# Kernel optimization log

Hardware: AMD Instinct MI355X
Metric: run time of the kernel (lower is better)

Reference implementation:

```python
import jax, jax.numpy as jnp
import numpy as np

R = 3          # bilateral radius -> 7x7 window (kernel_size=7, dilation=1)
NIC = 12       # num_input_channels per frame
NHS = 1        # num_hidden_states
DN = ('NCHW', 'OIHW', 'NCHW')


def _conv(x, w, b, groups=1):
    y = jax.lax.conv_general_dilated(x, w, (1, 1), 'SAME',
                                     dimension_numbers=DN,
                                     feature_group_count=groups)
    return y + b[None, :, None, None]


def _lcn(x, k=3):
    # run_lcn(color, 3): local contrast normalization with k x k box window, per channel
    C = x.shape[1]
    box = jnp.ones((C, 1, k, k), x.dtype) / (k * k)
    zb = jnp.zeros((C,), x.dtype)
    mean = _conv(x, box, zb, groups=C)
    mean2 = _conv(x * x, box, zb, groups=C)
    var = jnp.maximum(mean2 - mean * mean, 0.0)
    return (x - mean) * jax.lax.rsqrt(var + 1e-5)


def _bilateral(dyn, feat, scale):
    # cross-bilateral: weights from guide features, applied to dynamic channels
    B, _, H, W = dyn.shape
    pad = ((0, 0), (0, 0), (R, R), (R, R))
    fp = jnp.pad(feat, pad, mode='edge')
    dp = jnp.pad(dyn, pad, mode='edge')
    s = scale[None, :, None, None]            # [1,8,1,1] per-feature inverse sigma^2
    acc = jnp.zeros_like(dyn)
    wsum = jnp.zeros((B, 1, H, W), dyn.dtype)
    for dy in range(2 * R + 1):
        for dx in range(2 * R + 1):
            fq = fp[:, :, dy:dy + H, dx:dx + W]
            w = jnp.exp(-jnp.sum(s * (feat - fq) ** 2, axis=1, keepdims=True))
            acc = acc + w * dp[:, :, dy:dy + H, dx:dx + W]
            wsum = wsum + w
    return acc / (wsum + 1e-8)


def _forward(x, alpha, cr_w0, cr_b0, cr_w1, cr_b1, cr_w2, cr_b2,
             hs_w0, hs_b0, hs_w1, hs_b1, hs_w2, hs_b2,
             filt_w, filt_b, filt_scale):
    B, CT, H, W = x.shape
    num_frames = CT // NIC
    a = alpha[0]
    temporal = jnp.zeros((B, 3 + NHS, H, W), x.dtype)
    outs = []
    for i in range(num_frames):
        frame = x[:, i * NIC:(i + 1) * NIC]
        color, albedo, fixed = frame[:, :3], frame[:, 3:6], frame[:, 3:]
        rec_in = jnp.concatenate([_lcn(color), color], axis=1)           # 6ch
        h = jax.nn.relu(_conv(rec_in, cr_w0, cr_b0))
        h = jax.nn.relu(_conv(h, cr_w1, cr_b1))
        recombined = _conv(h, cr_w2, cr_b2)                              # 3ch
        hs_in = jnp.concatenate([recombined, fixed], axis=1)             # 12ch
        h = jax.nn.relu(_conv(hs_in, hs_w0, hs_b0))
        h = jax.nn.relu(_conv(h, hs_w1, hs_b1))
        hidden = _conv(h, hs_w2, hs_b2)                                  # 1ch
        dynamic = jnp.concatenate([color, hidden], axis=1)               # 4ch
        if i != 0:
            dynamic = a * dynamic + (1.0 - a) * temporal
        filtered = jnp.concatenate([dynamic, fixed], axis=1)             # 13ch
        for k in range(5):
            feat = _conv(filtered, filt_w[k], filt_b[k])                 # 8 guide features
            fdyn = _bilateral(filtered[:, :3 + NHS], feat, filt_scale[k])
            filtered = jnp.concatenate([fdyn, fixed], axis=1)
        outs.append(albedo * filtered[:, :3])
        temporal = filtered[:, :3 + NHS]
    return jnp.concatenate(outs, axis=1)   # [B, 3*num_frames, H, W]


def setup_inputs():
    key = jax.random.key(0)
    ks = jax.random.split(key, 12)
    w = lambda k, s: (0.1 * jax.random.normal(k, s)).astype(jnp.float32)
    z = lambda s: jnp.zeros(s, jnp.float32)
    return {
        'x': jax.random.normal(ks[0], (1, 48, 720, 1280), dtype=jnp.float32),
        'alpha': jnp.full((1,), 0.5, jnp.float32),
        'cr_w0': w(ks[1], (6, 6, 3, 3)),   'cr_b0': z((6,)),
        'cr_w1': w(ks[2], (12, 6, 3, 3)),  'cr_b1': z((12,)),
        'cr_w2': w(ks[3], (3, 12, 3, 3)),  'cr_b2': z((3,)),
        'hs_w0': w(ks[4], (12, 12, 3, 3)), 'hs_b0': z((12,)),
        'hs_w1': w(ks[5], (12, 12, 3, 3)), 'hs_b1': z((12,)),
        'hs_w2': w(ks[6], (1, 12, 3, 3)),  'hs_b2': z((1,)),
        'filt_w': w(ks[7], (5, 8, 13, 3, 3)), 'filt_b': z((5, 8)),
        'filt_scale': 0.5 * jax.random.uniform(ks[8], (5, 8), dtype=jnp.float32),
    }


def reference(x, alpha, cr_w0, cr_b0, cr_w1, cr_b1, cr_w2, cr_b2,
              hs_w0, hs_b0, hs_w1, hs_b1, hs_w2, hs_b2,
              filt_w, filt_b, filt_scale):
    return _forward(x, alpha, cr_w0, cr_b0, cr_w1, cr_b1, cr_w2, cr_b2,
                    hs_w0, hs_b0, hs_w1, hs_b1, hs_w2, hs_b2,
                    filt_w, filt_b, filt_scale)
```

## Files before the change

kernel.cpp:

```cpp
#include <hip/hip_runtime.h>

#define HH 720
#define WW 1280
#define HWP (HH*WW)

static constexpr int NFRM = 4;
typedef _Float16 h2 __attribute__((ext_vector_type(2)));

template <int PX, int C0, int C1, int COUT, bool RELU>
__global__ __launch_bounds__(128) void conv3x3_v3(const float* __restrict__ in0, long i0fs,
                                                  const float* __restrict__ in1, long i1fs,
                                                  const float* __restrict__ w,
                                                  const float* __restrict__ b,
                                                  float* __restrict__ out, long ofs) {
  constexpr int CIN = C0 + C1;
  constexpr int NBX = WW / (16 * PX);
  int fi = blockIdx.y;
  in0 += (size_t)fi * i0fs;
  out += (size_t)fi * ofs;
  const float* in1f = nullptr;
  if constexpr (C1 > 0) in1f = in1 + (size_t)fi * i1fs;

  int bx = blockIdx.x % NBX;
  int by = blockIdx.x / NBX;
  int tx = threadIdx.x & 15;
  int ty = threadIdx.x >> 4;
  int gx0 = bx * (16 * PX) + tx * PX;
  int gy  = by * 8 + ty;

  float acc[COUT][PX];
  #pragma unroll
  for (int co = 0; co < COUT; ++co) {
    float bv = b[co];
    #pragma unroll
    for (int px = 0; px < PX; ++px) acc[co][px] = bv;
  }

  const bool lok = (gx0 > 0);
  const bool rok = (gx0 + PX < WW);

  for (int c = 0; c < CIN; ++c) {
    const float* ch;
    if constexpr (C1 > 0)
      ch = (c < C0) ? (in0 + (size_t)c * HWP) : (in1f + (size_t)(c - C0) * HWP);
    else
      ch = in0 + (size_t)c * HWP;
    float r[3][PX + 2];
    #pragma unroll
    for (int ky = 0; ky < 3; ++ky) {
      int iy = gy + ky - 1;
      bool yok = (iy >= 0) && (iy < HH);
      const float* row = ch + (ptrdiff_t)iy * WW;
      #pragma unroll
      for (int j = 0; j < PX / 4; ++j) {
        float4 a = yok ? *reinterpret_cast<const float4*>(row + gx0 + 4 * j)
                       : make_float4(0.f, 0.f, 0.f, 0.f);
        r[ky][1 + 4*j + 0] = a.x; r[ky][1 + 4*j + 1] = a.y;
        r[ky][1 + 4*j + 2] = a.z; r[ky][1 + 4*j + 3] = a.w;
      }
      r[ky][0]      = (yok && lok) ? row[gx0 - 1]  : 0.f;
      r[ky][PX + 1] = (yok && rok) ? row[gx0 + PX] : 0.f;
    }
    #pragma unroll
    for (int co = 0; co < COUT; ++co) {
      #pragma unroll
      for (int ky = 0; ky < 3; ++ky) {
        #pragma unroll
        for (int kx = 0; kx < 3; ++kx) {
          float wv = w[((co * CIN + c) * 3 + ky) * 3 + kx];
          #pragma unroll
          for (int px = 0; px < PX; ++px)
            acc[co][px] = fmaf(wv, r[ky][px + kx], acc[co][px]);
        }
      }
    }
  }

  size_t p = (size_t)gy * WW + gx0;
  #pragma unroll
  for (int co = 0; co < COUT; ++co) {
    #pragma unroll
    for (int j = 0; j < PX / 4; ++j) {
      float4 o;
      o.x = RELU ? fmaxf(acc[co][4*j+0], 0.f) : acc[co][4*j+0];
      o.y = RELU ? fmaxf(acc[co][4*j+1], 0.f) : acc[co][4*j+1];
      o.z = RELU ? fmaxf(acc[co][4*j+2], 0.f) : acc[co][4*j+2];
      o.w = RELU ? fmaxf(acc[co][4*j+3], 0.f) : acc[co][4*j+3];
      *reinterpret_cast<float4*>(out + (size_t)co * HWP + p + 4*j) = o;
    }
  }
}

__global__ __launch_bounds__(128) void lcn_v3(const float* __restrict__ x, long ifs,
                                              float* __restrict__ out, long ofs) {
  constexpr int NBX = WW / 128;
  int fi = blockIdx.y;
  const float* color = x + (size_t)fi * ifs;
  out += (size_t)fi * ofs;
  int bx = blockIdx.x % NBX;
  int by = blockIdx.x / NBX;
  int tx = threadIdx.x & 15;
  int ty = threadIdx.x >> 4;
  int gx0 = bx * 128 + tx * 8;
  int gy  = by * 8 + ty;
  const bool lok = (gx0 > 0);
  const bool rok = (gx0 + 8 < WW);
  size_t p = (size_t)gy * WW + gx0;

  #pragma unroll
  for (int c = 0; c < 3; ++c) {
    const float* ch = color + (size_t)c * HWP;
    float r[3][10];
    #pragma unroll
    for (int ky = 0; ky < 3; ++ky) {
      int iy = gy + ky - 1;
      bool yok = (iy >= 0) && (iy < HH);
      const float* row = ch + (ptrdiff_t)iy * WW;
      float4 a = yok ? *reinterpret_cast<const float4*>(row + gx0)
                     : make_float4(0.f, 0.f, 0.f, 0.f);
      float4 q = yok ? *reinterpret_cast<const float4*>(row + gx0 + 4)
                     : make_float4(0.f, 0.f, 0.f, 0.f);
      r[ky][0] = (yok && lok) ? row[gx0 - 1] : 0.f;
      r[ky][1] = a.x; r[ky][2] = a.y; r[ky][3] = a.z; r[ky][4] = a.w;
      r[ky][5] = q.x; r[ky][6] = q.y; r[ky][7] = q.z; r[ky][8] = q.w;
      r[ky][9] = (yok && rok) ? row[gx0 + 8] : 0.f;
    }
    float lcnv[8], cv[8];
    #pragma unroll
    for (int px = 0; px < 8; ++px) {
      float s = 0.f, s2 = 0.f;
      #pragma unroll
      for (int ky = 0; ky < 3; ++ky)
        #pragma unroll
        for (int kx = 0; kx < 3; ++kx) {
          float v = r[ky][px + kx];
          s += v; s2 = fmaf(v, v, s2);
        }
      float mean = s * (1.f / 9.f);
      float mean2 = s2 * (1.f / 9.f);
      float var = fmaxf(mean2 - mean * mean, 0.f);
      cv[px] = r[1][px + 1];
      lcnv[px] = (cv[px] - mean) * rsqrtf(var + 1e-5f);
    }
    #pragma unroll
    for (int h = 0; h < 2; ++h) {
      float4 o0 = make_float4(lcnv[4*h+0], lcnv[4*h+1], lcnv[4*h+2], lcnv[4*h+3]);
      float4 o1 = make_float4(cv[4*h+0], cv[4*h+1], cv[4*h+2], cv[4*h+3]);
      *reinterpret_cast<float4*>(out + (size_t)c * HWP + p + 4*h) = o0;
      *reinterpret_cast<float4*>(out + (size_t)(3 + c) * HWP + p + 4*h) = o1;
    }
  }
}

__global__ __launch_bounds__(256) void blend_v3(const float* __restrict__ color,
                                                const float* __restrict__ hid,
                                                const float* __restrict__ temporal,
                                                const float* __restrict__ alpha,
                                                float* __restrict__ dyn, int first) {
  int i = (blockIdx.x * 256 + threadIdx.x) * 4;
  if (i >= HWP) return;
  if (first) {
    #pragma unroll
    for (int c = 0; c < 3; ++c)
      *reinterpret_cast<float4*>(dyn + (size_t)c * HWP + i) =
          *reinterpret_cast<const float4*>(color + (size_t)c * HWP + i);
    *reinterpret_cast<float4*>(dyn + 3 * (size_t)HWP + i) =
        *reinterpret_cast<const float4*>(hid + i);
  } else {
    float a = alpha[0];
    float om = 1.f - a;
    #pragma unroll
    for (int c = 0; c < 4; ++c) {
      const float* src = (c < 3) ? (color + (size_t)c * HWP) : hid;
      float4 cv = *reinterpret_cast<const float4*>(src + i);
      float4 tv = *reinterpret_cast<const float4*>(temporal + (size_t)c * HWP + i);
      float4 o;
      o.x = a * cv.x + om * tv.x;
      o.y = a * cv.y + om * tv.y;
      o.z = a * cv.z + om * tv.z;
      o.w = a * cv.w + om * tv.w;
      *reinterpret_cast<float4*>(dyn + (size_t)c * HWP + i) = o;
    }
  }
}

#define BC 38
#define BR 22
#define BNPX (BC*BR)
#define BPAD 840

__device__ __forceinline__ int bswz(int lin) { return lin ^ ((lin >> 3) & 7); }
__device__ __forceinline__ unsigned pkh(float a, float b) {
  return __builtin_bit_cast(unsigned, __builtin_amdgcn_cvt_pkrtz(a, b));
}

template <bool OUT>
__global__ __launch_bounds__(256, 4) void bilateral_v5(const float* __restrict__ dyn,
                                                       const float* __restrict__ feat,
                                                       const float* __restrict__ scale,
                                                       float* __restrict__ outdyn,
                                                       const float* __restrict__ albedo,
                                                       float* __restrict__ outp) {
  __shared__ uint4  ft[BPAD];
  __shared__ float4 dt[BPAD];
  int bx = blockIdx.x % 40;
  int by = blockIdx.x / 40;
  int tid = threadIdx.x;

  for (int i = tid; i < BNPX; i += 256) {
    int py = i / BC;
    int px = i - py * BC;
    int gy = min(max(by * 16 + py - 3, 0), HH - 1);
    int gx = min(max(bx * 32 + px - 3, 0), WW - 1);
    size_t g = (size_t)gy * WW + gx;
    int w = bswz(i);
    dt[w] = make_float4(dyn[g], dyn[HWP + g], dyn[2*(size_t)HWP + g], dyn[3*(size_t)HWP + g]);
    uint4 u;
    u.x = pkh(feat[g],                 feat[HWP + g]);
    u.y = pkh(feat[2*(size_t)HWP + g], feat[3*(size_t)HWP + g]);
    u.z = pkh(feat[4*(size_t)HWP + g], feat[5*(size_t)HWP + g]);
    u.w = pkh(feat[6*(size_t)HWP + g], feat[7*(size_t)HWP + g]);
    ft[w] = u;
  }
  __syncthreads();

  int txg = tid & 15;
  int ty  = tid >> 4;

  float sv[8];
  #pragma unroll
  for (int c = 0; c < 8; ++c) sv[c] = scale[c];

  float sfc[2][8], A[2];
  #pragma unroll
  for (int p = 0; p < 2; ++p) {
    int lin = (ty + 3) * BC + txg * 2 + 3 + p;
    uint4 u = ft[bswz(lin)];
    h2 a0 = __builtin_bit_cast(h2, u.x), a1 = __builtin_bit_cast(h2, u.y);
    h2 a2 = __builtin_bit_cast(h2, u.z), a3 = __builtin_bit_cast(h2, u.w);
    float fc[8] = {(float)a0[0], (float)a0[1], (float)a1[0], (float)a1[1],
                   (float)a2[0], (float)a2[1], (float)a3[0], (float)a3[1]};
    float aa = 0.f;
    #pragma unroll
    for (int c = 0; c < 8; ++c) {
      sfc[p][c] = sv[c] * fc[c];
      aa = fmaf(sfc[p][c], fc[c], aa);
    }
    A[p] = aa;
  }

  float acc[2][4], ws2[2];
  #pragma unroll
  for (int p = 0; p < 2; ++p) {
    ws2[p] = 0.f;
    acc[p][0] = acc[p][1] = acc[p][2] = acc[p][3] = 0.f;
  }

  for (int dy = 0; dy < 7; ++dy) {
    int rowb = (ty + dy) * BC + txg * 2;
    #pragma unroll
    for (int dx = 0; dx < 8; ++dx) {
      int w = bswz(rowb + dx);
      float4 dv = dt[w];
      uint4 u = ft[w];
      h2 a0 = __builtin_bit_cast(h2, u.x), a1 = __builtin_bit_cast(h2, u.y);
      h2 a2 = __builtin_bit_cast(h2, u.z), a3 = __builtin_bit_cast(h2, u.w);
      float f[8] = {(float)a0[0], (float)a0[1], (float)a1[0], (float)a1[1],
                    (float)a2[0], (float)a2[1], (float)a3[0], (float)a3[1]};
      float B = 0.f;
      #pragma unroll
      for (int c = 0; c < 8; ++c) B = fmaf(sv[c] * f[c], f[c], B);
      #pragma unroll
      for (int p = 0; p < 2; ++p) {
        if (dx - p >= 0 && dx - p <= 6) {
          float C = 0.f;
          #pragma unroll
          for (int c = 0; c < 8; ++c) C = fmaf(sfc[p][c], f[c], C);
          float e = fmaf(-2.f, C, A[p] + B);
          float wgt = __expf(-e);
          acc[p][0] = fmaf(wgt, dv.x, acc[p][0]);
          acc[p][1] = fmaf(wgt, dv.y, acc[p][1]);
          acc[p][2] = fmaf(wgt, dv.z, acc[p][2]);
          acc[p][3] = fmaf(wgt, dv.w, acc[p][3]);
          ws2[p] += wgt;
        }
      }
    }
  }

  int gy = by * 16 + ty;
  int gx0 = bx * 32 + txg * 2;
  size_t p0 = (size_t)gy * WW + gx0;
  float inv0 = 1.f / (ws2[0] + 1e-8f);
  float inv1 = 1.f / (ws2[1] + 1e-8f);
  #pragma unroll
  for (int c = 0; c < 4; ++c) {
    float2 o = make_float2(acc[0][c] * inv0, acc[1][c] * inv1);
    *reinterpret_cast<float2*>(outdyn + (size_t)c * HWP + p0) = o;
    if (OUT && c < 3) {
      float2 al = *reinterpret_cast<const float2*>(albedo + (size_t)c * HWP + p0);
      float2 oo = make_float2(o.x * al.x, o.y * al.y);
      *reinterpret_cast<float2*>(outp + (size_t)c * HWP + p0) = oo;
    }
  }
}

extern "C" void kernel_launch(void* const* d_in, const int* in_sizes, int n_in,
                              void* d_out, int out_size, void* d_ws, size_t ws_size,
                              hipStream_t stream) {
  const float* x          = (const float*)d_in[0];
  const float* alpha      = (const float*)d_in[1];
  const float* cr_w0      = (const float*)d_in[2];
  const float* cr_b0      = (const float*)d_in[3];
  const float* cr_w1      = (const float*)d_in[4];
  const float* cr_b1      = (const float*)d_in[5];
  const float* cr_w2      = (const float*)d_in[6];
  const float* cr_b2      = (const float*)d_in[7];
  const float* hs_w0      = (const float*)d_in[8];
  const float* hs_b0      = (const float*)d_in[9];
  const float* hs_w1      = (const float*)d_in[10];
  const float* hs_b1      = (const float*)d_in[11];
  const float* hs_w2      = (const float*)d_in[12];
  const float* hs_b2      = (const float*)d_in[13];
  const float* filt_w     = (const float*)d_in[14];
  const float* filt_b     = (const float*)d_in[15];
  const float* filt_scale = (const float*)d_in[16];

  float* out = (float*)d_out;
  float* ws  = (float*)d_ws;
  const size_t P = (size_t)HWP;

  bool batched = ws_size >= (size_t)108 * P * sizeof(float);
  float *bufA, *bufB, *dynT, *dynA, *dynB, *hid, *feat;
  if (batched) {
    bufA = ws;            bufB = ws + 48 * P;
    dynT = ws + 96 * P;   dynA = ws + 100 * P;  dynB = ws + 104 * P;
  } else {
    bufA = ws;            bufB = ws + 12 * P;
    dynT = ws + 24 * P;   dynA = ws + 28 * P;   dynB = ws + 32 * P;
  }
  hid  = bufA;
  feat = bufB;

  const int NB8 = (WW / 128) * (HH / 8);
  const int NB4 = (WW / 64)  * (HH / 8);
  const int NBE = HWP / (256 * 4);
  const int NBB = (WW / 32)  * (HH / 16);

  if (batched) {
    dim3 g8(NB8, NFRM), g4(NB4, NFRM);
    lcn_v3<<<g8, 128, 0, stream>>>(x, 12 * P, bufA, 6 * P);
    conv3x3_v3<4, 6, 0, 6,  true ><<<g4, 128, 0, stream>>>(bufA, 6 * P,  nullptr, 0, cr_w0, cr_b0, bufB, 6 * P);
    conv3x3_v3<4, 6, 0, 12, true ><<<g4, 128, 0, stream>>>(bufB, 6 * P,  nullptr, 0, cr_w1, cr_b1, bufA, 12 * P);
    conv3x3_v3<4, 12, 0, 3, false><<<g4, 128, 0, stream>>>(bufA, 12 * P, nullptr, 0, cr_w2, cr_b2, bufB, 3 * P);
    conv3x3_v3<4, 3, 9, 12, true ><<<g4, 128, 0, stream>>>(bufB, 3 * P,  x + 3 * P, 12 * P, hs_w0, hs_b0, bufA, 12 * P);
    conv3x3_v3<4, 12, 0, 12, true><<<g4, 128, 0, stream>>>(bufA, 12 * P, nullptr, 0, hs_w1, hs_b1, bufB, 12 * P);
    conv3x3_v3<4, 12, 0, 1, false><<<g4, 128, 0, stream>>>(bufB, 12 * P, nullptr, 0, hs_w2, hs_b2, hid, P);
  }

  for (int f = 0; f < NFRM; ++f) {
    const float* frame  = x + (size_t)f * 12 * P;
    const float* fixedp = frame + 3 * P;

    if (!batched) {
      dim3 g8(NB8, 1), g4(NB4, 1);
      lcn_v3<<<g8, 128, 0, stream>>>(frame, 0, bufA, 0);
      conv3x3_v3<4, 6, 0, 6,  true ><<<g4, 128, 0, stream>>>(bufA, 0, nullptr, 0, cr_w0, cr_b0, bufB, 0);
      conv3x3_v3<4, 6, 0, 12, true ><<<g4, 128, 0, stream>>>(bufB, 0, nullptr, 0, cr_w1, cr_b1, bufA, 0);
      conv3x3_v3<4, 12, 0, 3, false><<<g4, 128, 0, stream>>>(bufA, 0, nullptr, 0, cr_w2, cr_b2, bufB, 0);
      conv3x3_v3<4, 3, 9, 12, true ><<<g4, 128, 0, stream>>>(bufB, 0, fixedp, 0, hs_w0, hs_b0, bufA, 0);
      conv3x3_v3<4, 12, 0, 12, true><<<g4, 128, 0, stream>>>(bufA, 0, nullptr, 0, hs_w1, hs_b1, bufB, 0);
      conv3x3_v3<4, 12, 0, 1, false><<<g4, 128, 0, stream>>>(bufB, 0, nullptr, 0, hs_w2, hs_b2, hid, 0);
    }

    const float* hidf = batched ? (hid + (size_t)f * P) : hid;
    blend_v3<<<NBE, 256, 0, stream>>>(frame, hidf, dynT, alpha, dynA, f == 0 ? 1 : 0);

    float* cur = dynA;
    float* nxt = dynB;
    for (int k = 0; k < 5; ++k) {
      conv3x3_v3<4, 4, 9, 8, false><<<dim3(NB4, 1), 128, 0, stream>>>(
          cur, 0, fixedp, 0, filt_w + (size_t)k * 8 * 13 * 9, filt_b + k * 8, feat, 0);
      const float* sk = filt_scale + k * 8;
      if (k < 4) {
        bilateral_v5<false><<<NBB, 256, 0, stream>>>(cur, feat, sk, nxt, nullptr, nullptr);
        float* t = cur; cur = nxt; nxt = t;
      } else {
        bilateral_v5<true><<<NBB, 256, 0, stream>>>(cur, feat, sk, dynT,
                                                    fixedp, out + (size_t)f * 3 * P);
      }
    }
  }
}
```

Baseline: 2.543 ms.

## Store CNN intermediate activations in fp16 and raise bilateral occupancy hint

LCN output and the recombiner and hidden-state CNN intermediates are now stored in half precision, and the conv kernel is templated on input and output types. This roughly halves the memory traffic of the per-frame CNN stages and shrinks the workspace, so the batched path needs less scratch memory. Accumulation stays fp32. The bilateral kernel's launch bounds min-blocks hint is raised from 4 to 6. FP16 storage adds rounding error to the hidden state and the recombined color, and the tighter register budget could cause spills in the bilateral kernel.

```diff
diff --git a/kernel.cpp b/kernel.cpp
--- a/kernel.cpp
+++ b/kernel.cpp
@@ -7,18 +7,62 @@
 static constexpr int NFRM = 4;
 typedef _Float16 h2 __attribute__((ext_vector_type(2)));
 
-template <int PX, int C0, int C1, int COUT, bool RELU>
-__global__ __launch_bounds__(128) void conv3x3_v3(const float* __restrict__ in0, long i0fs,
-                                                  const float* __restrict__ in1, long i1fs,
-                                                  const float* __restrict__ w,
-                                                  const float* __restrict__ b,
-                                                  float* __restrict__ out, long ofs) {
+template <int PX>
+__device__ __forceinline__ void ldrow(const float* __restrict__ row, int gx0,
+                                      bool yok, bool lok, bool rok, float* r) {
+  if (yok) {
+    #pragma unroll
+    for (int j = 0; j < PX / 4; ++j) {
+      float4 a = *reinterpret_cast<const float4*>(row + gx0 + 4 * j);
+      r[1 + 4*j] = a.x; r[2 + 4*j] = a.y; r[3 + 4*j] = a.z; r[4 + 4*j] = a.w;
+    }
+    r[0]      = lok ? row[gx0 - 1]  : 0.f;
+    r[PX + 1] = rok ? row[gx0 + PX] : 0.f;
+  } else {
+    #pragma unroll
+    for (int j = 0; j < PX + 2; ++j) r[j] = 0.f;
+  }
+}
+
+template <int PX>
+__device__ __forceinline__ void ldrow(const _Float16* __restrict__ row, int gx0,
+                                      bool yok, bool lok, bool rok, float* r) {
+  if (yok) {
+    #pragma unroll
+    for (int j = 0; j < PX / 2; ++j) {
+      h2 a = *reinterpret_cast<const h2*>(row + gx0 + 2 * j);
+      r[1 + 2*j] = (float)a[0]; r[2 + 2*j] = (float)a[1];
+    }
+    r[0]      = lok ? (float)row[gx0 - 1]  : 0.f;
+    r[PX + 1] = rok ? (float)row[gx0 + PX] : 0.f;
+  } else {
+    #pragma unroll
+    for (int j = 0; j < PX + 2; ++j) r[j] = 0.f;
+  }
+}
+
+__device__ __forceinline__ void st4(float* o, size_t p, float a, float b, float c, float d) {
+  *reinterpret_cast<float4*>(o + p) = make_float4(a, b, c, d);
+}
+__device__ __forceinline__ void st4(_Float16* o, size_t p, float a, float b, float c, float d) {
+  h2 u; u[0] = (_Float16)a; u[1] = (_Float16)b;
+  h2 v; v[0] = (_Float16)c; v[1] = (_Float16)d;
+  *reinterpret_cast<h2*>(o + p)     = u;
+  *reinterpret_cast<h2*>(o + p + 2) = v;
+}
+
+template <int PX, int C0, int C1, int COUT, bool RELU, typename T0, typename T1, typename TO>
+__global__ __launch_bounds__(128) void conv_h(const T0* __restrict__ in0, long i0fs,
+                                              const T1* __restrict__ in1, long i1fs,
+                                              const float* __restrict__ w,
+                                              const float* __restrict__ b,
+                                              TO* __restrict__ out, long ofs) {
   constexpr int CIN = C0 + C1;
   constexpr int NBX = WW / (16 * PX);
   int fi = blockIdx.y;
   in0 += (size_t)fi * i0fs;
   out += (size_t)fi * ofs;
-  const float* in1f = nullptr;
+  const T1* in1f = nullptr;
   if constexpr (C1 > 0) in1f = in1 + (size_t)fi * i1fs;
 
   int bx = blockIdx.x % NBX;
@@ -39,41 +83,44 @@
   const bool lok = (gx0 > 0);
   const bool rok = (gx0 + PX < WW);
 
-  for (int c = 0; c < CIN; ++c) {
-    const float* ch;
-    if constexpr (C1 > 0)
-      ch = (c < C0) ? (in0 + (size_t)c * HWP) : (in1f + (size_t)(c - C0) * HWP);
-    else
-      ch = in0 + (size_t)c * HWP;
-    float r[3][PX + 2];
-    #pragma unroll
-    for (int ky = 0; ky < 3; ++ky) {
-      int iy = gy + ky - 1;
-      bool yok = (iy >= 0) && (iy < HH);
-      const float* row = ch + (ptrdiff_t)iy * WW;
-      #pragma unroll
-      for (int j = 0; j < PX / 4; ++j) {
-        float4 a = yok ? *reinterpret_cast<const float4*>(row + gx0 + 4 * j)
-                       : make_float4(0.f, 0.f, 0.f, 0.f);
-        r[ky][1 + 4*j + 0] = a.x; r[ky][1 + 4*j + 1] = a.y;
-        r[ky][1 + 4*j + 2] = a.z; r[ky][1 + 4*j + 3] = a.w;
-      }
-      r[ky][0]      = (yok && lok) ? row[gx0 - 1]  : 0.f;
-      r[ky][PX + 1] = (yok && rok) ? row[gx0 + PX] : 0.f;
-    }
+  float r[3][PX + 2];
+  auto mac = [&](int cw) {
     #pragma unroll
     for (int co = 0; co < COUT; ++co) {
       #pragma unroll
       for (int ky = 0; ky < 3; ++ky) {
         #pragma unroll
         for (int kx = 0; kx < 3; ++kx) {
-          float wv = w[((co * CIN + c) * 3 + ky) * 3 + kx];
+          float wv = w[((co * CIN + cw) * 3 + ky) * 3 + kx];
           #pragma unroll
           for (int px = 0; px < PX; ++px)
             acc[co][px] = fmaf(wv, r[ky][px + kx], acc[co][px]);
         }
       }
     }
+  };
+
+  for (int c = 0; c < C0; ++c) {
+    const T0* ch = in0 + (size_t)c * HWP;
+    #pragma unroll
+    for (int ky = 0; ky < 3; ++ky) {
+      int iy = gy + ky - 1;
+      bool yok = (iy >= 0) && (iy < HH);
+      ldrow<PX>(ch + (ptrdiff_t)iy * WW, gx0, yok, lok, rok, r[ky]);
+    }
+    mac(c);
+  }
+  if constexpr (C1 > 0) {
+    for (int c = 0; c < C1; ++c) {
+      const T1* ch = in1f + (size_t)c * HWP;
+      #pragma unroll
+      for (int ky = 0; ky < 3; ++ky) {
+        int iy = gy + ky - 1;
+        bool yok = (iy >= 0) && (iy < HH);
+        ldrow<PX>(ch + (ptrdiff_t)iy * WW, gx0, yok, lok, rok, r[ky]);
+      }
+      mac(C0 + c);
+    }
   }
 
   size_t p = (size_t)gy * WW + gx0;
@@ -81,18 +128,17 @@
   for (int co = 0; co < COUT; ++co) {
     #pragma unroll
     for (int j = 0; j < PX / 4; ++j) {
-      float4 o;
-      o.x = RELU ? fmaxf(acc[co][4*j+0], 0.f) : acc[co][4*j+0];
-      o.y = RELU ? fmaxf(acc[co][4*j+1], 0.f) : acc[co][4*j+1];
-      o.z = RELU ? fmaxf(acc[co][4*j+2], 0.f) : acc[co][4*j+2];
-      o.w = RELU ? fmaxf(acc[co][4*j+3], 0.f) : acc[co][4*j+3];
-      *reinterpret_cast<float4*>(out + (size_t)co * HWP + p + 4*j) = o;
-    }
-  }
-}
-
-__global__ __launch_bounds__(128) void lcn_v3(const float* __restrict__ x, long ifs,
-                                              float* __restrict__ out, long ofs) {
+      float o0 = RELU ? fmaxf(acc[co][4*j+0], 0.f) : acc[co][4*j+0];
+      float o1 = RELU ? fmaxf(acc[co][4*j+1], 0.f) : acc[co][4*j+1];
+      float o2 = RELU ? fmaxf(acc[co][4*j+2], 0.f) : acc[co][4*j+2];
+      float o3 = RELU ? fmaxf(acc[co][4*j+3], 0.f) : acc[co][4*j+3];
+      st4(out + (size_t)co * HWP, p + 4*j, o0, o1, o2, o3);
+    }
+  }
+}
+
+__global__ __launch_bounds__(128) void lcn_h(const float* __restrict__ x, long ifs,
+                                             _Float16* __restrict__ out, long ofs) {
   constexpr int NBX = WW / 128;
   int fi = blockIdx.y;
   const float* color = x + (size_t)fi * ifs;
@@ -115,15 +161,7 @@
     for (int ky = 0; ky < 3; ++ky) {
       int iy = gy + ky - 1;
       bool yok = (iy >= 0) && (iy < HH);
-      const float* row = ch + (ptrdiff_t)iy * WW;
-      float4 a = yok ? *reinterpret_cast<const float4*>(row + gx0)
-                     : make_float4(0.f, 0.f, 0.f, 0.f);
-      float4 q = yok ? *reinterpret_cast<const float4*>(row + gx0 + 4)
-                     : make_float4(0.f, 0.f, 0.f, 0.f);
-      r[ky][0] = (yok && lok) ? row[gx0 - 1] : 0.f;
-      r[ky][1] = a.x; r[ky][2] = a.y; r[ky][3] = a.z; r[ky][4] = a.w;
-      r[ky][5] = q.x; r[ky][6] = q.y; r[ky][7] = q.z; r[ky][8] = q.w;
-      r[ky][9] = (yok && rok) ? row[gx0 + 8] : 0.f;
+      ldrow<8>(ch + (ptrdiff_t)iy * WW, gx0, yok, lok, rok, r[ky]);
     }
     float lcnv[8], cv[8];
     #pragma unroll
@@ -142,37 +180,40 @@
       cv[px] = r[1][px + 1];
       lcnv[px] = (cv[px] - mean) * rsqrtf(var + 1e-5f);
     }
-    #pragma unroll
-    for (int h = 0; h < 2; ++h) {
-      float4 o0 = make_float4(lcnv[4*h+0], lcnv[4*h+1], lcnv[4*h+2], lcnv[4*h+3]);
-      float4 o1 = make_float4(cv[4*h+0], cv[4*h+1], cv[4*h+2], cv[4*h+3]);
-      *reinterpret_cast<float4*>(out + (size_t)c * HWP + p + 4*h) = o0;
-      *reinterpret_cast<float4*>(out + (size_t)(3 + c) * HWP + p + 4*h) = o1;
-    }
-  }
-}
-
-__global__ __launch_bounds__(256) void blend_v3(const float* __restrict__ color,
-                                                const float* __restrict__ hid,
+    _Float16* o0 = out + (size_t)c * HWP;
+    _Float16* o1 = out + (size_t)(3 + c) * HWP;
+    #pragma unroll
+    for (int h = 0; h < 4; ++h) {
+      h2 u; u[0] = (_Float16)lcnv[2*h]; u[1] = (_Float16)lcnv[2*h + 1];
+      h2 v; v[0] = (_Float16)cv[2*h];   v[1] = (_Float16)cv[2*h + 1];
+      *reinterpret_cast<h2*>(o0 + p + 2*h) = u;
+      *reinterpret_cast<h2*>(o1 + p + 2*h) = v;
+    }
+  }
+}
+
+__global__ __launch_bounds__(256) void blend_v4(const float* __restrict__ color,
+                                                const _Float16* __restrict__ hid,
                                                 const float* __restrict__ temporal,
                                                 const float* __restrict__ alpha,
                                                 float* __restrict__ dyn, int first) {
   int i = (blockIdx.x * 256 + threadIdx.x) * 4;
   if (i >= HWP) return;
+  h2 ha = *reinterpret_cast<const h2*>(hid + i);
+  h2 hb = *reinterpret_cast<const h2*>(hid + i + 2);
+  float4 hv = make_float4((float)ha[0], (float)ha[1], (float)hb[0], (float)hb[1]);
   if (first) {
     #pragma unroll
     for (int c = 0; c < 3; ++c)
       *reinterpret_cast<float4*>(dyn + (size_t)c * HWP + i) =
           *reinterpret_cast<const float4*>(color + (size_t)c * HWP + i);
-    *reinterpret_cast<float4*>(dyn + 3 * (size_t)HWP + i) =
-        *reinterpret_cast<const float4*>(hid + i);
+    *reinterpret_cast<float4*>(dyn + 3 * (size_t)HWP + i) = hv;
   } else {
     float a = alpha[0];
     float om = 1.f - a;
     #pragma unroll
     for (int c = 0; c < 4; ++c) {
-      const float* src = (c < 3) ? (color + (size_t)c * HWP) : hid;
-      float4 cv = *reinterpret_cast<const float4*>(src + i);
+      float4 cv = (c < 3) ? *reinterpret_cast<const float4*>(color + (size_t)c * HWP + i) : hv;
       float4 tv = *reinterpret_cast<const float4*>(temporal + (size_t)c * HWP + i);
       float4 o;
       o.x = a * cv.x + om * tv.x;
@@ -195,7 +236,7 @@
 }
 
 template <bool OUT>
-__global__ __launch_bounds__(256, 4) void bilateral_v5(const float* __restrict__ dyn,
+__global__ __launch_bounds__(256, 6) void bilateral_v5(const float* __restrict__ dyn,
                                                        const float* __restrict__ feat,
                                                        const float* __restrict__ scale,
                                                        float* __restrict__ outdyn,
@@ -330,56 +371,63 @@
   float* ws  = (float*)d_ws;
   const size_t P = (size_t)HWP;
 
-  bool batched = ws_size >= (size_t)108 * P * sizeof(float);
-  float *bufA, *bufB, *dynT, *dynA, *dynB, *hid, *feat;
+  bool batched = ws_size >= (size_t)68 * P * sizeof(float);
+  _Float16 *b16A, *b16B;
+  float *dynT, *dynA, *dynB, *feat;
+  long sA, sB;
   if (batched) {
-    bufA = ws;            bufB = ws + 48 * P;
-    dynT = ws + 96 * P;   dynA = ws + 100 * P;  dynB = ws + 104 * P;
+    b16A = (_Float16*)ws;
+    b16B = (_Float16*)(ws + 24 * P);
+    dynT = ws + 48 * P;  dynA = ws + 52 * P;  dynB = ws + 56 * P;
+    feat = ws + 60 * P;
   } else {
-    bufA = ws;            bufB = ws + 12 * P;
-    dynT = ws + 24 * P;   dynA = ws + 28 * P;   dynB = ws + 32 * P;
-  }
-  hid  = bufA;
-  feat = bufB;
+    b16A = (_Float16*)ws;
+    b16B = (_Float16*)(ws + 6 * P);
+    dynT = ws + 12 * P;  dynA = ws + 16 * P;  dynB = ws + 20 * P;
+    feat = ws + 24 * P;
+  }
+  _Float16* hid16 = b16A;
 
   const int NB8 = (WW / 128) * (HH / 8);
   const int NB4 = (WW / 64)  * (HH / 8);
   const int NBE = HWP / (256 * 4);
   const int NBB = (WW / 32)  * (HH / 16);
 
-  if (batched) {
-    dim3 g8(NB8, NFRM), g4(NB4, NFRM);
-    lcn_v3<<<g8, 128, 0, stream>>>(x, 12 * P, bufA, 6 * P);
-    conv3x3_v3<4, 6, 0, 6,  true ><<<g4, 128, 0, stream>>>(bufA, 6 * P,  nullptr, 0, cr_w0, cr_b0, bufB, 6 * P);
-    conv3x3_v3<4, 6, 0, 12, true ><<<g4, 128, 0, stream>>>(bufB, 6 * P,  nullptr, 0, cr_w1, cr_b1, bufA, 12 * P);
-    conv3x3_v3<4, 12, 0, 3, false><<<g4, 128, 0, stream>>>(bufA, 12 * P, nullptr, 0, cr_w2, cr_b2, bufB, 3 * P);
-    conv3x3_v3<4, 3, 9, 12, true ><<<g4, 128, 0, stream>>>(bufB, 3 * P,  x + 3 * P, 12 * P, hs_w0, hs_b0, bufA, 12 * P);
-    conv3x3_v3<4, 12, 0, 12, true><<<g4, 128, 0, stream>>>(bufA, 12 * P, nullptr, 0, hs_w1, hs_b1, bufB, 12 * P);
-    conv3x3_v3<4, 12, 0, 1, false><<<g4, 128, 0, stream>>>(bufB, 12 * P, nullptr, 0, hs_w2, hs_b2, hid, P);
-  }
+  const int NF = batched ? NFRM : 1;
+  dim3 g8(NB8, NF), g4(NB4, NF);
+  long x12 = batched ? 12 * (long)P : 0;
+
+  auto run_cnn = [&](const float* xin) {
+    lcn_h<<<g8, 128, 0, stream>>>(xin, x12, b16A, batched ? 6 * (long)P : 0);
+    conv_h<4, 6, 0, 6,  true , _Float16, float, _Float16><<<g4, 128, 0, stream>>>(
+        b16A, batched ? 6 * (long)P : 0, nullptr, 0, cr_w0, cr_b0, b16B, batched ? 6 * (long)P : 0);
+    conv_h<4, 6, 0, 12, true , _Float16, float, _Float16><<<g4, 128, 0, stream>>>(
+        b16B, batched ? 6 * (long)P : 0, nullptr, 0, cr_w1, cr_b1, b16A, batched ? 12 * (long)P : 0);
+    conv_h<4, 12, 0, 3, false, _Float16, float, _Float16><<<g4, 128, 0, stream>>>(
+        b16A, batched ? 12 * (long)P : 0, nullptr, 0, cr_w2, cr_b2, b16B, batched ? 3 * (long)P : 0);
+    conv_h<4, 3, 9, 12, true , _Float16, float, _Float16><<<g4, 128, 0, stream>>>(
+        b16B, batched ? 3 * (long)P : 0, xin + 3 * P, x12, hs_w0, hs_b0, b16A, batched ? 12 * (long)P : 0);
+    conv_h<4, 12, 0, 12, true, _Float16, float, _Float16><<<g4, 128, 0, stream>>>(
+        b16A, batched ? 12 * (long)P : 0, nullptr, 0, hs_w1, hs_b1, b16B, batched ? 12 * (long)P : 0);
+    conv_h<4, 12, 0, 1, false, _Float16, float, _Float16><<<g4, 128, 0, stream>>>(
+        b16B, batched ? 12 * (long)P : 0, nullptr, 0, hs_w2, hs_b2, b16A, batched ? (long)P : 0);
+  };
+
+  if (batched) run_cnn(x);
 
   for (int f = 0; f < NFRM; ++f) {
     const float* frame  = x + (size_t)f * 12 * P;
     const float* fixedp = frame + 3 * P;
 
-    if (!batched) {
-      dim3 g8(NB8, 1), g4(NB4, 1);
-      lcn_v3<<<g8, 128, 0, stream>>>(frame, 0, bufA, 0);
-      conv3x3_v3<4, 6, 0, 6,  true ><<<g4, 128, 0, stream>>>(bufA, 0, nullptr, 0, cr_w0, cr_b0, bufB, 0);
-      conv3x3_v3<4, 6, 0, 12, true ><<<g4, 128, 0, stream>>>(bufB, 0, nullptr, 0, cr_w1, cr_b1, bufA, 0);
-      conv3x3_v3<4, 12, 0, 3, false><<<g4, 128, 0, stream>>>(bufA, 0, nullptr, 0, cr_w2, cr_b2, bufB, 0);
-      conv3x3_v3<4, 3, 9, 12, true ><<<g4, 128, 0, stream>>>(bufB, 0, fixedp, 0, hs_w0, hs_b0, bufA, 0);
-      conv3x3_v3<4, 12, 0, 12, true><<<g4, 128, 0, stream>>>(bufA, 0, nullptr, 0, hs_w1, hs_b1, bufB, 0);
-      conv3x3_v3<4, 12, 0, 1, false><<<g4, 128, 0, stream>>>(bufB, 0, nullptr, 0, hs_w2, hs_b2, hid, 0);
-    }
-
-    const float* hidf = batched ? (hid + (size_t)f * P) : hid;
-    blend_v3<<<NBE, 256, 0, stream>>>(frame, hidf, dynT, alpha, dynA, f == 0 ? 1 : 0);
+    if (!batched) run_cnn(frame);
+
+    const _Float16* hidf = batched ? (hid16 + (size_t)f * P) : hid16;
+    blend_v4<<<NBE, 256, 0, stream>>>(frame, hidf, dynT, alpha, dynA, f == 0 ? 1 : 0);
 
     float* cur = dynA;
     float* nxt = dynB;
     for (int k = 0; k < 5; ++k) {
-      conv3x3_v3<4, 4, 9, 8, false><<<dim3(NB4, 1), 128, 0, stream>>>(
+      conv_h<4, 4, 9, 8, false, float, float, float><<<dim3(NB4, 1), 128, 0, stream>>>(
           cur, 0, fixedp, 0, filt_w + (size_t)k * 8 * 13 * 9, filt_b + k * 8, feat, 0);
       const float* sk = filt_scale + k * 8;
       if (k < 4) {
```

After: 3.279 ms. 1.29x slower.
